# Kernel optimization log

Hardware: AMD Instinct MI355X
Metric: run time of the kernel (lower is better)

The kernel has to match this reference:

```python
import jax, jax.numpy as jnp
import numpy as np

N_NODES = 100000
N_EDGES = 1600000
D_IN = 64
D_OUT = 64
EDGE_DIM = 16


def setup_inputs() -> dict:
    key = jax.random.key(0)
    ks = jax.random.split(key, 6)
    x = jax.random.normal(ks[0], (N_NODES, D_IN), dtype=jnp.float32)
    edge_index = jax.random.randint(ks[1], (2, N_EDGES), 0, N_NODES, dtype=jnp.int64)
    edge_feature = jax.random.normal(ks[2], (N_EDGES, EDGE_DIM), dtype=jnp.float32)
    W_edge = jax.random.normal(ks[3], (EDGE_DIM, 1), dtype=jnp.float32) * (1.0 / np.sqrt(EDGE_DIM))
    b_edge = jnp.zeros((1,), dtype=jnp.float32)
    W_node = jax.random.normal(ks[4], (D_OUT, D_IN), dtype=jnp.float32) * (1.0 / np.sqrt(D_IN))
    b_node = jnp.zeros((D_OUT,), dtype=jnp.float32)
    return {"x": x, "edge_index": edge_index, "edge_feature": edge_feature,
            "W_edge": W_edge, "b_edge": b_edge, "W_node": W_node, "b_node": b_node}


def reference(x, edge_index, edge_feature, W_edge, b_edge, W_node, b_node):
    # per-edge gate: Linear(edge_dim -> 1) + Sigmoid  -> [E]
    gate = jax.nn.sigmoid(edge_feature @ W_edge + b_edge)[:, 0]
    # node projection: Linear(in -> out)  -> [N, D_OUT]
    xp = x @ W_node.T + b_node
    row = edge_index[0]  # destination (SparseTensor row)
    col = edge_index[1]  # source gathered
    num_nodes = x.shape[0]
    # weighted gather of source node features  -> [E, D_OUT]
    msg = gate[:, None] * xp[col]
    summed = jax.ops.segment_sum(msg, row, num_segments=num_nodes)
    cnt = jax.ops.segment_sum(jnp.ones((row.shape[0],), dtype=xp.dtype), row,
                              num_segments=num_nodes)
    # reduce='mean': divide by row nnz count; empty rows stay 0
    out = summed / jnp.maximum(cnt, 1.0)[:, None]
    return out
```

## Files before the change

### kernel.cpp

```cpp
#include <hip/hip_runtime.h>
#include <math.h>

#define NN 100000
#define NE 1600000
#define DD 64
#define ED 16
#define BROWS 96
#define NBIN 1042
#define NBIN_PAD 1056
#define BCAP 1920
#define EPB 8192
#define NBLKA ((NE + EPB - 1) / EPB)


__device__ __forceinline__ unsigned short f2bf(float f) {
    unsigned int b = __float_as_uint(f);
    unsigned int r = (b + 0x7FFFu + ((b >> 16) & 1u)) >> 16;
    return (unsigned short)r;
}

__global__ __launch_bounds__(256) void proj_kernel(
    const float* __restrict__ x, const float* __restrict__ Wn,
    const float* __restrict__ bn, unsigned short* __restrict__ xpb,
    int* __restrict__ cursor) {
    __shared__ float xs[128][66];
    __shared__ float ws[64][66];
    int tid = threadIdx.x;
    if (blockIdx.x == 0) {
        for (int i = tid; i < NBIN_PAD; i += 256) cursor[i] = i * BCAP;
    }
    int n0 = blockIdx.x * 128;
    const float4* x4 = reinterpret_cast<const float4*>(x);
    const float4* Wn4 = reinterpret_cast<const float4*>(Wn);
    long limit = (long)NN * 16;
#pragma unroll
    for (int i = 0; i < 8; ++i) {
        int idx = tid + 256 * i;
        int row = idx >> 4, kq = idx & 15;
        long gidx = (long)n0 * 16 + idx;
        float4 v = (gidx < limit) ? x4[gidx] : make_float4(0.f, 0.f, 0.f, 0.f);
        xs[row][kq * 4 + 0] = v.x; xs[row][kq * 4 + 1] = v.y;
        xs[row][kq * 4 + 2] = v.z; xs[row][kq * 4 + 3] = v.w;
    }
#pragma unroll
    for (int i = 0; i < 4; ++i) {
        int idx = tid + 256 * i;
        int row = idx >> 4, kq = idx & 15;
        float4 v = Wn4[idx];
        ws[row][kq * 4 + 0] = v.x; ws[row][kq * 4 + 1] = v.y;
        ws[row][kq * 4 + 2] = v.z; ws[row][kq * 4 + 3] = v.w;
    }
    int og = tid & 15;
    int ng = tid >> 4;
    float acc[8][4];
    float b0 = bn[og * 4 + 0], b1 = bn[og * 4 + 1];
    float b2 = bn[og * 4 + 2], b3 = bn[og * 4 + 3];
#pragma unroll
    for (int i = 0; i < 8; ++i) {
        acc[i][0] = b0; acc[i][1] = b1; acc[i][2] = b2; acc[i][3] = b3;
    }
    __syncthreads();
#pragma unroll 4
    for (int kk = 0; kk < 32; ++kk) {
        float2 wv0 = *reinterpret_cast<const float2*>(&ws[og * 4 + 0][kk * 2]);
        float2 wv1 = *reinterpret_cast<const float2*>(&ws[og * 4 + 1][kk * 2]);
        float2 wv2 = *reinterpret_cast<const float2*>(&ws[og * 4 + 2][kk * 2]);
        float2 wv3 = *reinterpret_cast<const float2*>(&ws[og * 4 + 3][kk * 2]);
#pragma unroll
        for (int i = 0; i < 8; ++i) {
            float2 xv = *reinterpret_cast<const float2*>(&xs[ng * 8 + i][kk * 2]);
            acc[i][0] += xv.x * wv0.x + xv.y * wv0.y;
            acc[i][1] += xv.x * wv1.x + xv.y * wv1.y;
            acc[i][2] += xv.x * wv2.x + xv.y * wv2.y;
            acc[i][3] += xv.x * wv3.x + xv.y * wv3.y;
        }
    }
#pragma unroll
    for (int i = 0; i < 8; ++i) {
        int n = n0 + ng * 8 + i;
        if (n < NN) {
            ushort4 o;
            o.x = f2bf(acc[i][0]); o.y = f2bf(acc[i][1]);
            o.z = f2bf(acc[i][2]); o.w = f2bf(acc[i][3]);
            *reinterpret_cast<ushort4*>(xpb + (size_t)n * DD + og * 4) = o;
        }
    }
}

__global__ __launch_bounds__(256) void gate_kernel(
    const float* __restrict__ ef, const float* __restrict__ We,
    const float* __restrict__ be, unsigned short* __restrict__ g16) {
    int e = blockIdx.x * 256 + threadIdx.x;
    if (e >= NE) return;
    const float4* ef4 = reinterpret_cast<const float4*>(ef + (size_t)e * ED);
    const float4* We4 = reinterpret_cast<const float4*>(We);
    float4 a0 = ef4[0], a1 = ef4[1], a2 = ef4[2], a3 = ef4[3];
    float4 w0 = We4[0], w1 = We4[1], w2 = We4[2], w3 = We4[3];
    float d = a0.x * w0.x + a0.y * w0.y + a0.z * w0.z + a0.w * w0.w
            + a1.x * w1.x + a1.y * w1.y + a1.z * w1.z + a1.w * w1.w
            + a2.x * w2.x + a2.y * w2.y + a2.z * w2.z + a2.w * w2.w
            + a3.x * w3.x + a3.y * w3.y + a3.z * w3.z + a3.w * w3.w + be[0];
    float g = 1.f / (1.f + expf(-d));
    int q = (int)(g * 65535.f + 0.5f);
    g16[e] = (unsigned short)min(q, 65535);
}

__global__ __launch_bounds__(1024) void binA_kernel(
    const int* __restrict__ ei, const unsigned short* __restrict__ g16,
    int* __restrict__ cursor, int2* __restrict__ binned) {
    __shared__ int cnt[NBIN_PAD];
    __shared__ int basev[NBIN_PAD];
    int tid = threadIdx.x;
    int e0 = blockIdx.x * EPB;
    cnt[tid] = 0;
    if (tid < NBIN_PAD - 1024) cnt[tid + 1024] = 0;
    __syncthreads();
    int e_base = e0 + tid * 8;
    bool ok = e_base < NE;
    int4 ra, rb, ca, cb;
    ushort4 ga, gb;
    int s0=0,s1=0,s2=0,s3=0,s4=0,s5=0,s6=0,s7=0;
    int b0=0,b1=0,b2=0,b3=0,b4=0,b5=0,b6=0,b7=0;
    if (ok) {
        const int4* pr = reinterpret_cast<const int4*>(ei + e_base);
        ra = pr[0]; rb = pr[1];
        const int4* pc = reinterpret_cast<const int4*>(ei + NE + e_base);
        ca = pc[0]; cb = pc[1];
        const ushort4* pg = reinterpret_cast<const ushort4*>(g16 + e_base);
        ga = pg[0]; gb = pg[1];
        b0 = ra.x / BROWS; s0 = atomicAdd(&cnt[b0], 1);
        b1 = ra.y / BROWS; s1 = atomicAdd(&cnt[b1], 1);
        b2 = ra.z / BROWS; s2 = atomicAdd(&cnt[b2], 1);
        b3 = ra.w / BROWS; s3 = atomicAdd(&cnt[b3], 1);
        b4 = rb.x / BROWS; s4 = atomicAdd(&cnt[b4], 1);
        b5 = rb.y / BROWS; s5 = atomicAdd(&cnt[b5], 1);
        b6 = rb.z / BROWS; s6 = atomicAdd(&cnt[b6], 1);
        b7 = rb.w / BROWS; s7 = atomicAdd(&cnt[b7], 1);
    }
    __syncthreads();
    for (int i = tid; i < NBIN_PAD; i += 1024) {
        int c = cnt[i];
        basev[i] = c ? atomicAdd(&cursor[i], c) : 0;
    }
    __syncthreads();
    if (ok) {
        const float gs = 1.f / 65535.f;
#define EMIT(BV, SV, RR, CC, GG) \
        binned[basev[BV] + SV] = make_int2((((RR) - (BV) * BROWS) << 24) | (CC), \
                                           __float_as_int((float)(GG) * gs));
        EMIT(b0, s0, ra.x, ca.x, ga.x) EMIT(b1, s1, ra.y, ca.y, ga.y)
        EMIT(b2, s2, ra.z, ca.z, ga.z) EMIT(b3, s3, ra.w, ca.w, ga.w)
        EMIT(b4, s4, rb.x, cb.x, gb.x) EMIT(b5, s5, rb.y, cb.y, gb.y)
        EMIT(b6, s6, rb.z, cb.z, gb.z) EMIT(b7, s7, rb.w, cb.w, gb.w)
#undef EMIT
    }
}

__global__ __launch_bounds__(512) void binB_kernel(
    const unsigned short* __restrict__ xpb, const int* __restrict__ cursor,
    const int2* __restrict__ binned, float* __restrict__ out) {
    __shared__ int2 sorted[BCAP];
    __shared__ int hist[128];
    __shared__ int offs[128];
    __shared__ int claim[BROWS];
    int tid = threadIdx.x;
    int b = blockIdx.x;
    if (tid < 128) { hist[tid] = 0; offs[tid] = 0; }
    if (tid < BROWS) claim[tid] = 0;
    __syncthreads();
    int bstart = b * BCAP;
    int nb = cursor[b] - bstart;
    for (int t = tid; t < nb; t += 512) {
        int w = binned[bstart + t].x;
        atomicAdd(&hist[(w >> 24) & 0x7F], 1);
    }
    __syncthreads();
    if (tid < 128) offs[tid] = hist[tid];
    __syncthreads();
    for (int d = 1; d < 128; d <<= 1) {
        int add = 0;
        if (tid < 128 && tid >= d) add = offs[tid - d];
        __syncthreads();
        if (tid < 128) offs[tid] += add;
        __syncthreads();
    }
    for (int t = tid; t < nb; t += 512) {
        int2 e = binned[bstart + t];
        int rl = (e.x >> 24) & 0x7F;
        int pos = offs[rl] - hist[rl] + atomicAdd(&claim[rl], 1);
        sorted[pos] = e;
    }
    __syncthreads();
    int lane = tid & 63;
    int wv = tid >> 6;
    int half = lane >> 5;
    int hl = lane & 31;
#pragma unroll 1
    for (int i = 0; i < 12; ++i) {
        int rl = wv + 8 * i;
        int row = b * BROWS + rl;
        if (row >= NN) break;
        int dn = hist[rl];
        int s0 = offs[rl] - dn;
        float ax = 0.f, ay = 0.f;
        for (int j = 0; j < dn; j += 16) {
#pragma unroll
            for (int k = 0; k < 8; ++k) {
                int ei_ = j + 2 * k + half;
                int2 e = sorted[s0 + min(ei_, dn - 1)];
                float g = (ei_ < dn) ? __int_as_float(e.y) : 0.f;
                int col = e.x & 0x1FFFF;
                unsigned int u = *reinterpret_cast<const unsigned int*>(
                    xpb + (size_t)col * DD + 2 * hl);
                ax += g * __uint_as_float(u << 16);
                ay += g * __uint_as_float(u & 0xFFFF0000u);
            }
        }
        ax += __shfl_xor(ax, 32);
        ay += __shfl_xor(ay, 32);
        if (half == 0) {
            float dv = fmaxf((float)dn, 1.f);
            reinterpret_cast<float2*>(out)[(size_t)row * 32 + hl] =
                make_float2(ax / dv, ay / dv);
        }
    }
}

extern "C" void kernel_launch(void* const* d_in, const int* in_sizes, int n_in,
                              void* d_out, int out_size, void* d_ws, size_t ws_size,
                              hipStream_t stream) {
    const float* x  = (const float*)d_in[0];
    const int*   ei = (const int*)d_in[1];
    const float* ef = (const float*)d_in[2];
    const float* We = (const float*)d_in[3];
    const float* be = (const float*)d_in[4];
    const float* Wn = (const float*)d_in[5];
    const float* bn = (const float*)d_in[6];
    float* out = (float*)d_out;

    unsigned short* xpb = (unsigned short*)d_ws;
    int*  cursor = (int*)d_ws + 3200000;
    unsigned short* g16 = (unsigned short*)((int*)d_ws + 3201056);
    int2* binned = (int2*)((int*)d_ws + 4001056);

    proj_kernel<<<(NN + 127) / 128, 256, 0, stream>>>(x, Wn, bn, xpb, cursor);
    gate_kernel<<<(NE + 255) / 256, 256, 0, stream>>>(ef, We, be, g16);
    binA_kernel<<<NBLKA, 1024, 0, stream>>>(ei, g16, cursor, binned);
    binB_kernel<<<NBIN, 512, 0, stream>>>(xpb, cursor, binned, out);
}
```

Before: 116.4 us.

## Fuse gate computation into binning kernel and widen gather per lane

Removes the separate gate kernel and computes the sigmoid edge gate inside the binning kernel. This avoids the 16-bit gate round trip through global memory and one launch, and keeps the gate in full fp32 precision. The binning kernel now uses 512 threads with 4 edges per thread over smaller edge chunks, giving more blocks and more global cursor atomics. The aggregation kernel now has each lane load 4 bf16 values, with quarter-wave edge parallelism and a two-step shuffle reduction and float4 stores.

```diff
diff --git a/kernel.cpp b/kernel.cpp
--- a/kernel.cpp
+++ b/kernel.cpp
@@ -9,7 +9,7 @@
 #define NBIN 1042
 #define NBIN_PAD 1056
 #define BCAP 1920
-#define EPB 8192
+#define EPB 2048
 #define NBLKA ((NE + EPB - 1) / EPB)
 
 
@@ -87,71 +87,60 @@
     }
 }
 
-__global__ __launch_bounds__(256) void gate_kernel(
-    const float* __restrict__ ef, const float* __restrict__ We,
-    const float* __restrict__ be, unsigned short* __restrict__ g16) {
-    int e = blockIdx.x * 256 + threadIdx.x;
-    if (e >= NE) return;
-    const float4* ef4 = reinterpret_cast<const float4*>(ef + (size_t)e * ED);
-    const float4* We4 = reinterpret_cast<const float4*>(We);
-    float4 a0 = ef4[0], a1 = ef4[1], a2 = ef4[2], a3 = ef4[3];
-    float4 w0 = We4[0], w1 = We4[1], w2 = We4[2], w3 = We4[3];
-    float d = a0.x * w0.x + a0.y * w0.y + a0.z * w0.z + a0.w * w0.w
-            + a1.x * w1.x + a1.y * w1.y + a1.z * w1.z + a1.w * w1.w
-            + a2.x * w2.x + a2.y * w2.y + a2.z * w2.z + a2.w * w2.w
-            + a3.x * w3.x + a3.y * w3.y + a3.z * w3.z + a3.w * w3.w + be[0];
-    float g = 1.f / (1.f + expf(-d));
-    int q = (int)(g * 65535.f + 0.5f);
-    g16[e] = (unsigned short)min(q, 65535);
-}
-
-__global__ __launch_bounds__(1024) void binA_kernel(
-    const int* __restrict__ ei, const unsigned short* __restrict__ g16,
+__global__ __launch_bounds__(512) void binAG_kernel(
+    const int* __restrict__ ei, const float* __restrict__ ef,
+    const float* __restrict__ We, const float* __restrict__ be,
     int* __restrict__ cursor, int2* __restrict__ binned) {
     __shared__ int cnt[NBIN_PAD];
     __shared__ int basev[NBIN_PAD];
     int tid = threadIdx.x;
     int e0 = blockIdx.x * EPB;
-    cnt[tid] = 0;
-    if (tid < NBIN_PAD - 1024) cnt[tid + 1024] = 0;
-    __syncthreads();
-    int e_base = e0 + tid * 8;
+    for (int i = tid; i < NBIN_PAD; i += 512) cnt[i] = 0;
+    __syncthreads();
+    int e_base = e0 + tid * 4;
     bool ok = e_base < NE;
-    int4 ra, rb, ca, cb;
-    ushort4 ga, gb;
-    int s0=0,s1=0,s2=0,s3=0,s4=0,s5=0,s6=0,s7=0;
-    int b0=0,b1=0,b2=0,b3=0,b4=0,b5=0,b6=0,b7=0;
+    int4 r, c;
+    float4 f0, f1, f2, f3, f4, f5, f6, f7, f8, f9, fa, fb, fc, fd, fe, ff;
+    int s0 = 0, s1 = 0, s2 = 0, s3 = 0;
+    int b0 = 0, b1 = 0, b2 = 0, b3 = 0;
     if (ok) {
-        const int4* pr = reinterpret_cast<const int4*>(ei + e_base);
-        ra = pr[0]; rb = pr[1];
-        const int4* pc = reinterpret_cast<const int4*>(ei + NE + e_base);
-        ca = pc[0]; cb = pc[1];
-        const ushort4* pg = reinterpret_cast<const ushort4*>(g16 + e_base);
-        ga = pg[0]; gb = pg[1];
-        b0 = ra.x / BROWS; s0 = atomicAdd(&cnt[b0], 1);
-        b1 = ra.y / BROWS; s1 = atomicAdd(&cnt[b1], 1);
-        b2 = ra.z / BROWS; s2 = atomicAdd(&cnt[b2], 1);
-        b3 = ra.w / BROWS; s3 = atomicAdd(&cnt[b3], 1);
-        b4 = rb.x / BROWS; s4 = atomicAdd(&cnt[b4], 1);
-        b5 = rb.y / BROWS; s5 = atomicAdd(&cnt[b5], 1);
-        b6 = rb.z / BROWS; s6 = atomicAdd(&cnt[b6], 1);
-        b7 = rb.w / BROWS; s7 = atomicAdd(&cnt[b7], 1);
-    }
-    __syncthreads();
-    for (int i = tid; i < NBIN_PAD; i += 1024) {
-        int c = cnt[i];
-        basev[i] = c ? atomicAdd(&cursor[i], c) : 0;
+        r = *reinterpret_cast<const int4*>(ei + e_base);
+        c = *reinterpret_cast<const int4*>(ei + NE + e_base);
+        const float4* p = reinterpret_cast<const float4*>(ef + (size_t)e_base * ED);
+        f0 = p[0];  f1 = p[1];  f2 = p[2];  f3 = p[3];
+        f4 = p[4];  f5 = p[5];  f6 = p[6];  f7 = p[7];
+        f8 = p[8];  f9 = p[9];  fa = p[10]; fb = p[11];
+        fc = p[12]; fd = p[13]; fe = p[14]; ff = p[15];
+        b0 = r.x / BROWS; s0 = atomicAdd(&cnt[b0], 1);
+        b1 = r.y / BROWS; s1 = atomicAdd(&cnt[b1], 1);
+        b2 = r.z / BROWS; s2 = atomicAdd(&cnt[b2], 1);
+        b3 = r.w / BROWS; s3 = atomicAdd(&cnt[b3], 1);
+    }
+    __syncthreads();
+    for (int i = tid; i < NBIN_PAD; i += 512) {
+        int cc = cnt[i];
+        basev[i] = cc ? atomicAdd(&cursor[i], cc) : 0;
     }
     __syncthreads();
     if (ok) {
-        const float gs = 1.f / 65535.f;
+        const float4* We4 = reinterpret_cast<const float4*>(We);
+        float4 w0 = We4[0], w1 = We4[1], w2 = We4[2], w3 = We4[3];
+        float bb = be[0];
+#define DOT(A0, A1, A2, A3) \
+        (A0.x*w0.x + A0.y*w0.y + A0.z*w0.z + A0.w*w0.w + \
+         A1.x*w1.x + A1.y*w1.y + A1.z*w1.z + A1.w*w1.w + \
+         A2.x*w2.x + A2.y*w2.y + A2.z*w2.z + A2.w*w2.w + \
+         A3.x*w3.x + A3.y*w3.y + A3.z*w3.z + A3.w*w3.w + bb)
+        float g0 = 1.f / (1.f + expf(-DOT(f0, f1, f2, f3)));
+        float g1 = 1.f / (1.f + expf(-DOT(f4, f5, f6, f7)));
+        float g2 = 1.f / (1.f + expf(-DOT(f8, f9, fa, fb)));
+        float g3 = 1.f / (1.f + expf(-DOT(fc, fd, fe, ff)));
+#undef DOT
 #define EMIT(BV, SV, RR, CC, GG) \
-        binned[basev[BV] + SV] = make_int2((((RR) - (BV) * BROWS) << 24) | (CC), \
-                                           __float_as_int((float)(GG) * gs));
-        EMIT(b0, s0, ra.x, ca.x, ga.x) EMIT(b1, s1, ra.y, ca.y, ga.y)
-        EMIT(b2, s2, ra.z, ca.z, ga.z) EMIT(b3, s3, ra.w, ca.w, ga.w)
-        EMIT(b4, s4, rb.x, cb.x, gb.x) EMIT(b5, s5, rb.y, cb.y, gb.y)
-        EMIT(b6, s6, rb.z, cb.z, gb.z) EMIT(b7, s7, rb.w, cb.w, gb.w)
+        binned[basev[BV] + SV] = \
+            make_int2((((RR) - (BV) * BROWS) << 24) | (CC), __float_as_int(GG));
+        EMIT(b0, s0, r.x, c.x, g0) EMIT(b1, s1, r.y, c.y, g1)
+        EMIT(b2, s2, r.z, c.z, g2) EMIT(b3, s3, r.w, c.w, g3)
 #undef EMIT
     }
 }
@@ -193,8 +182,8 @@
     __syncthreads();
     int lane = tid & 63;
     int wv = tid >> 6;
-    int half = lane >> 5;
-    int hl = lane & 31;
+    int q = lane >> 4;
+    int ql = lane & 15;
 #pragma unroll 1
     for (int i = 0; i < 12; ++i) {
         int rl = wv + 8 * i;
@@ -202,26 +191,30 @@
         if (row >= NN) break;
         int dn = hist[rl];
         int s0 = offs[rl] - dn;
-        float ax = 0.f, ay = 0.f;
+        float a0 = 0.f, a1 = 0.f, a2 = 0.f, a3 = 0.f;
         for (int j = 0; j < dn; j += 16) {
 #pragma unroll
-            for (int k = 0; k < 8; ++k) {
-                int ei_ = j + 2 * k + half;
-                int2 e = sorted[s0 + min(ei_, dn - 1)];
-                float g = (ei_ < dn) ? __int_as_float(e.y) : 0.f;
+            for (int k = 0; k < 4; ++k) {
+                int idx = j + 4 * k + q;
+                int2 e = sorted[s0 + min(idx, dn - 1)];
+                float g = (idx < dn) ? __int_as_float(e.y) : 0.f;
                 int col = e.x & 0x1FFFF;
-                unsigned int u = *reinterpret_cast<const unsigned int*>(
-                    xpb + (size_t)col * DD + 2 * hl);
-                ax += g * __uint_as_float(u << 16);
-                ay += g * __uint_as_float(u & 0xFFFF0000u);
+                uint2 u = *reinterpret_cast<const uint2*>(
+                    xpb + (size_t)col * DD + ql * 4);
+                a0 += g * __uint_as_float(u.x << 16);
+                a1 += g * __uint_as_float(u.x & 0xFFFF0000u);
+                a2 += g * __uint_as_float(u.y << 16);
+                a3 += g * __uint_as_float(u.y & 0xFFFF0000u);
             }
         }
-        ax += __shfl_xor(ax, 32);
-        ay += __shfl_xor(ay, 32);
-        if (half == 0) {
+        a0 += __shfl_xor(a0, 16); a0 += __shfl_xor(a0, 32);
+        a1 += __shfl_xor(a1, 16); a1 += __shfl_xor(a1, 32);
+        a2 += __shfl_xor(a2, 16); a2 += __shfl_xor(a2, 32);
+        a3 += __shfl_xor(a3, 16); a3 += __shfl_xor(a3, 32);
+        if (q == 0) {
             float dv = fmaxf((float)dn, 1.f);
-            reinterpret_cast<float2*>(out)[(size_t)row * 32 + hl] =
-                make_float2(ax / dv, ay / dv);
+            *reinterpret_cast<float4*>(&out[(size_t)row * DD + ql * 4]) =
+                make_float4(a0 / dv, a1 / dv, a2 / dv, a3 / dv);
         }
     }
 }
@@ -240,11 +233,9 @@
 
     unsigned short* xpb = (unsigned short*)d_ws;
     int*  cursor = (int*)d_ws + 3200000;
-    unsigned short* g16 = (unsigned short*)((int*)d_ws + 3201056);
-    int2* binned = (int2*)((int*)d_ws + 4001056);
+    int2* binned = (int2*)((int*)d_ws + 3201056);
 
     proj_kernel<<<(NN + 127) / 128, 256, 0, stream>>>(x, Wn, bn, xpb, cursor);
-    gate_kernel<<<(NE + 255) / 256, 256, 0, stream>>>(ef, We, be, g16);
-    binA_kernel<<<NBLKA, 1024, 0, stream>>>(ei, g16, cursor, binned);
+    binAG_kernel<<<NBLKA, 512, 0, stream>>>(ei, ef, We, be, cursor, binned);
     binB_kernel<<<NBIN, 512, 0, stream>>>(xpb, cursor, binned, out);
 }
```

Measured after the change: 116.6 us. About the same (+0.2%).
